# Kernel tuning notes

Hardware: AMD Instinct MI355X
Metric: run time of the kernel (lower is better)

The kernel has to match this reference:

```python
import jax, jax.numpy as jnp
import numpy as np

RPN_BATCHSIZE = 256
RPN_FG_FRACTION = 0.5
NEG_OVERLAP = 0.3
POS_OVERLAP = 0.7
STRIDE = 16
ALLOWED_BORDER = 0.0


def _whctrs(a):
    w = a[2] - a[0] + 1.0
    h = a[3] - a[1] + 1.0
    return w, h, a[0] + 0.5 * (w - 1.0), a[1] + 0.5 * (h - 1.0)


def _mkanchors(ws, hs, xc, yc):
    return np.stack([xc - 0.5 * (ws - 1.0), yc - 0.5 * (hs - 1.0),
                     xc + 0.5 * (ws - 1.0), yc + 0.5 * (hs - 1.0)], axis=1)


def _base_anchors(base_size=16, ratios=(0.5, 1.0, 2.0), scales=(8.0, 16.0, 32.0)):
    ratios = np.asarray(ratios, np.float64)
    scales = np.asarray(scales, np.float64)
    base = np.array([1.0, 1.0, base_size, base_size]) - 1.0
    w, h, xc, yc = _whctrs(base)
    size = w * h
    ws = np.round(np.sqrt(size / ratios))
    hs = np.round(ws * ratios)
    ratio_anchors = _mkanchors(ws, hs, xc, yc)
    out = []
    for ra in ratio_anchors:
        w2, h2, xc2, yc2 = _whctrs(ra)
        out.append(_mkanchors(w2 * scales, h2 * scales, xc2, yc2))
    return np.concatenate(out, axis=0).astype(np.float32)  # (9, 4)


def _shift_anchors(rr, cc, stride):
    base = jnp.asarray(_base_anchors())  # (9, 4)
    sx = jnp.arange(rr, dtype=jnp.float32) * stride
    sy = jnp.arange(cc, dtype=jnp.float32) * stride
    SX, SY = jnp.meshgrid(sx, sy)  # 'xy' indexing like keras meshgrid
    shifts = jnp.stack([SX.ravel(), SY.ravel(), SX.ravel(), SY.ravel()], axis=1)
    return (base[None, :, :] + shifts[:, None, :]).reshape(-1, 4)  # (rr*cc*9, 4)


def _overlap(a, b):
    # pairwise IoU with the +1 pixel convention of keras_rcnn.backend.overlap
    area_a = (a[:, 2] - a[:, 0] + 1.0) * (a[:, 3] - a[:, 1] + 1.0)  # (N,)
    area_b = (b[:, 2] - b[:, 0] + 1.0) * (b[:, 3] - b[:, 1] + 1.0)  # (G,)
    iw = jnp.maximum(jnp.minimum(a[:, None, 2], b[None, :, 2]) - jnp.maximum(a[:, None, 0], b[None, :, 0]) + 1.0, 0.0)
    ih = jnp.maximum(jnp.minimum(a[:, None, 3], b[None, :, 3]) - jnp.maximum(a[:, None, 1], b[None, :, 1]) + 1.0, 0.0)
    inter = iw * ih
    return inter / (area_a[:, None] + area_b[None, :] - inter)


def _subsample(labels, target_value, max_count, key):
    # Randomly demote entries with labels == target_value beyond max_count to -1.
    # Replaces the TF shuffle+scatter with a vectorized rank-based selection.
    is_t = labels == target_value
    pri = jnp.where(is_t, jax.random.uniform(key, labels.shape), -1.0)
    order = jnp.argsort(-pri)
    n = labels.shape[0]
    rank = jnp.zeros((n,), jnp.int32).at[order].set(jnp.arange(n, dtype=jnp.int32))
    drop = is_t & (rank >= max_count)
    return jnp.where(drop, -1.0, labels)


def _bbox_transform(ex, gt):
    ew = ex[:, 2] - ex[:, 0] + 1.0
    eh = ex[:, 3] - ex[:, 1] + 1.0
    ecx = ex[:, 0] + 0.5 * ew
    ecy = ex[:, 1] + 0.5 * eh
    gw = gt[:, 2] - gt[:, 0] + 1.0
    gh = gt[:, 3] - gt[:, 1] + 1.0
    gcx = gt[:, 0] + 0.5 * gw
    gcy = gt[:, 1] + 0.5 * gh
    dx = (gcx - ecx) / ew
    dy = (gcy - ecy) / eh
    dw = jnp.log(gw / ew)
    dh = jnp.log(gh / eh)
    return jnp.stack([dx, dy, dw, dh], axis=1)


def _forward(scores, gt_boxes, metadata):
    meta = metadata[0]
    gt = gt_boxes[0]
    rr, cc = scores.shape[1], scores.shape[2]
    anchors = _shift_anchors(rr, cc, STRIDE)
    n = anchors.shape[0]
    iou = _overlap(anchors, gt)  # (N, G), dominant memory traffic
    argmax_inds = jnp.argmax(iou, axis=1)        # best gt per anchor
    max_overlaps = jnp.max(iou, axis=1)
    gt_argmax_inds = jnp.argmax(iou, axis=0)     # best anchor per gt
    labels = jnp.full((n,), -1.0, jnp.float32)
    labels = jnp.where(max_overlaps < NEG_OVERLAP, 0.0, labels)
    # unique+scatter_add in the original just sets those positions to 1
    labels = labels.at[gt_argmax_inds].set(1.0)
    labels = jnp.where(max_overlaps >= POS_OVERLAP, 1.0, labels)
    kpos, kneg = jax.random.split(jax.random.key(42))
    num_fg = int(RPN_FG_FRACTION * RPN_BATCHSIZE)
    labels = _subsample(labels, 1.0, num_fg, kpos)
    num_bg = RPN_BATCHSIZE - jnp.sum(labels == 1.0)
    labels = _subsample(labels, 0.0, num_bg, kneg)
    gt_sel = gt[argmax_inds]  # (N, 4)
    targets = _bbox_transform(anchors, gt_sel)
    inside = ((anchors[:, 0] >= -ALLOWED_BORDER) & (anchors[:, 1] >= -ALLOWED_BORDER) &
              (anchors[:, 2] < ALLOWED_BORDER + meta[1]) & (anchors[:, 3] < ALLOWED_BORDER + meta[0]))
    labels = jnp.where(inside, labels, -1.0)
    return labels[None, :], targets[None, :, :]


def setup_inputs() -> dict:
    key = jax.random.key(0)
    k1, k2 = jax.random.split(key)
    rr = cc = 128
    num_anchors = 9
    g = 256
    scores = jnp.zeros((1, rr, cc, 2 * num_anchors), jnp.float32)
    xy1 = jax.random.uniform(k1, (g, 2), jnp.float32) * 1600.0
    wh = 32.0 + jax.random.uniform(k2, (g, 2), jnp.float32) * 416.0
    xy2 = jnp.minimum(xy1 + wh, 2047.0)
    gt_boxes = jnp.concatenate([xy1, xy2], axis=1)[None, :, :]
    metadata = jnp.array([[2048.0, 2048.0, 1.0]], jnp.float32)
    return {"scores": scores, "gt_boxes": gt_boxes, "metadata": metadata}


def reference(scores, gt_boxes, metadata):
    return _forward(scores, gt_boxes, metadata)
```

## Files before the change

### kernel.cpp

```cpp
#include <hip/hip_runtime.h>
#include <stdint.h>

#pragma clang fp contract(off)

#define N_ANCH 147456
#define HALF_N 73728u
#define NG 256
#define NBINS 4096
#define CAND_CAP 4096
#define K_POS 128u
#define RPN_BATCH 256u
#define PARTITIONABLE 1

struct TFOut { uint32_t x0, x1; };

__host__ __device__ constexpr TFOut threefry2x32(uint32_t k0, uint32_t k1,
                                                 uint32_t c0, uint32_t c1) {
  uint32_t ks[3] = {k0, k1, k0 ^ k1 ^ 0x1BD11BDAu};
  uint32_t x0 = c0 + ks[0];
  uint32_t x1 = c1 + ks[1];
  const uint32_t rotA[4] = {13u, 15u, 26u, 6u};
  const uint32_t rotB[4] = {17u, 29u, 16u, 24u};
#pragma unroll
  for (int g = 0; g < 5; ++g) {
#pragma unroll
    for (int r = 0; r < 4; ++r) {
      uint32_t ro = ((g & 1) == 0) ? rotA[r] : rotB[r];
      x0 += x1;
      x1 = (x1 << ro) | (x1 >> (32u - ro));
      x1 ^= x0;
    }
    x0 += ks[(g + 1) % 3];
    x1 += ks[(g + 2) % 3] + (uint32_t)(g + 1);
  }
  return TFOut{x0, x1};
}

#if PARTITIONABLE
constexpr TFOut SK0 = threefry2x32(0u, 42u, 0u, 0u);
constexpr TFOut SK1 = threefry2x32(0u, 42u, 0u, 1u);
constexpr uint32_t KPOS0 = SK0.x0, KPOS1 = SK0.x1;
constexpr uint32_t KNEG0 = SK1.x0, KNEG1 = SK1.x1;
#else
constexpr TFOut SA = threefry2x32(0u, 42u, 0u, 2u);
constexpr TFOut SB = threefry2x32(0u, 42u, 1u, 3u);
constexpr uint32_t KPOS0 = SA.x0, KPOS1 = SB.x0;
constexpr uint32_t KNEG0 = SA.x1, KNEG1 = SB.x1;
#endif

__device__ __forceinline__ uint32_t rand_m23(uint32_t k0, uint32_t k1, uint32_t i) {
#if PARTITIONABLE
  TFOut o = threefry2x32(k0, k1, 0u, i);
  return (o.x0 ^ o.x1) >> 9;
#else
  uint32_t lo = (i < HALF_N) ? i : i - HALF_N;
  TFOut o = threefry2x32(k0, k1, lo, lo + HALF_N);
  return ((i < HALF_N) ? o.x0 : o.x1) >> 9;
#endif
}

__device__ const float c_base[9][4] = {
  { -84.f,  -40.f,  99.f,  55.f}, {-176.f,  -88.f, 191.f, 103.f},
  {-360.f, -184.f, 375.f, 199.f}, { -56.f,  -56.f,  71.f,  71.f},
  {-120.f, -120.f, 135.f, 135.f}, {-248.f, -248.f, 263.f, 263.f},
  { -36.f,  -80.f,  51.f,  95.f}, { -80.f, -168.f,  95.f, 183.f},
  {-168.f, -344.f, 183.f, 359.f}
};

__device__ __forceinline__ void anchor_coords(int a, float* x1, float* y1,
                                              float* x2, float* y2) {
  int b = a % 9;
  int cell = a / 9;
  float sx = (float)((cell & 127) << 4);
  float sy = (float)((cell >> 7) << 4);
  *x1 = c_base[b][0] + sx;
  *y1 = c_base[b][1] + sy;
  *x2 = c_base[b][2] + sx;
  *y2 = c_base[b][3] + sy;
}

__global__ __launch_bounds__(256) void k_anchor(const float* __restrict__ gt,
                                                float* __restrict__ labels,
                                                float* __restrict__ targets) {
  __shared__ float4 s_gt[NG];
  __shared__ float s_area[NG];
  const int tid = threadIdx.x;
  float4 bb = ((const float4*)gt)[tid];
  s_gt[tid] = bb;
  s_area[tid] = (bb.z - bb.x + 1.0f) * (bb.w - bb.y + 1.0f);
  __syncthreads();
  const int a = blockIdx.x * 256 + tid;
  float ax1, ay1, ax2, ay2;
  anchor_coords(a, &ax1, &ay1, &ax2, &ay2);
  const float area_a = (ax2 - ax1 + 1.0f) * (ay2 - ay1 + 1.0f);
  float best = -1.0f;
  int bj = 0;
  for (int j = 0; j < NG; ++j) {
    float4 b = s_gt[j];
    float iw = fminf(ax2, b.z) - fmaxf(ax1, b.x) + 1.0f;
    iw = fmaxf(iw, 0.0f);
    float ih = fminf(ay2, b.w) - fmaxf(ay1, b.y) + 1.0f;
    ih = fmaxf(ih, 0.0f);
    float inter = iw * ih;
    float v = inter / (area_a + s_area[j] - inter);
    if (v > best) { best = v; bj = j; }
  }
  labels[a] = (best >= 0.7f) ? 1.0f : ((best < 0.3f) ? 0.0f : -1.0f);
  float4 g = s_gt[bj];
  float ew = ax2 - ax1 + 1.0f;
  float eh = ay2 - ay1 + 1.0f;
  float ecx = ax1 + 0.5f * ew;
  float ecy = ay1 + 0.5f * eh;
  float gw = g.z - g.x + 1.0f;
  float gh = g.w - g.y + 1.0f;
  float gcx = g.x + 0.5f * gw;
  float gcy = g.y + 0.5f * gh;
  float4 t;
  t.x = (gcx - ecx) / ew;
  t.y = (gcy - ecy) / eh;
  t.z = logf(gw / ew);
  t.w = logf(gh / eh);
  ((float4*)targets)[a] = t;
}

__global__ __launch_bounds__(256) void k_gtbest_sep(const float* __restrict__ gt,
                                                    float* __restrict__ labels) {
  __shared__ unsigned long long s_best[2][9];
  __shared__ unsigned long long s_k[9];
  const int j = blockIdx.x;
  const int tid = threadIdx.x;
  if (tid < 18) s_best[tid / 9][tid % 9] = 0ull;
  __syncthreads();
  float4 b = ((const float4*)gt)[j];
  const int axis = tid >> 7;
  const int p = tid & 127;
  const float shift = (float)(p << 4);
  const float lo = axis ? b.y : b.x;
  const float hi = axis ? b.w : b.z;
#pragma unroll
  for (int k = 0; k < 9; ++k) {
    const float a1 = c_base[k][axis] + shift;
    const float a2 = c_base[k][axis + 2] + shift;
    float ext = fminf(a2, hi) - fmaxf(a1, lo) + 1.0f;
    ext = fmaxf(ext, 0.0f);
    unsigned long long key =
        ((unsigned long long)__float_as_uint(ext) << 7)
      | (unsigned long long)(127 - p);
    atomicMax(&s_best[axis][k], key);
  }
  __syncthreads();
  if (tid < 9) {
    const int k = tid;
    unsigned long long kx = s_best[0][k], ky = s_best[1][k];
    float iw = __uint_as_float((uint32_t)(kx >> 7));
    float ih = __uint_as_float((uint32_t)(ky >> 7));
    int xs = 127 - (int)(kx & 127u);
    int ys = 127 - (int)(ky & 127u);
    float inter = iw * ih;
    float area_a = (c_base[k][2] - c_base[k][0] + 1.0f) *
                   (c_base[k][3] - c_base[k][1] + 1.0f);
    float area_b = (b.z - b.x + 1.0f) * (b.w - b.y + 1.0f);
    float v = inter / (area_a + area_b - inter);
    uint32_t a = (uint32_t)((ys * 128 + xs) * 9 + k);
    s_k[k] = ((unsigned long long)__float_as_uint(v) << 32)
           | (unsigned long long)(0xFFFFFFFFu - a);
  }
  __syncthreads();
  if (tid == 0) {
    unsigned long long best = s_k[0];
#pragma unroll
    for (int k = 1; k < 9; ++k) if (s_k[k] > best) best = s_k[k];
    int besta = (int)(0xFFFFFFFFu - (uint32_t)(best & 0xFFFFFFFFull));
    labels[besta] = 1.0f;
  }
}

__global__ __launch_bounds__(256) void k_hist(const float* __restrict__ labels,
                                              uint32_t* __restrict__ hp,
                                              uint32_t* __restrict__ hn) {
  const int a = blockIdx.x * 256 + threadIdx.x;
  float l = labels[a];
  if (l == 1.0f) {
    atomicAdd(&hp[rand_m23(KPOS0, KPOS1, (uint32_t)a) >> 11], 1u);
  } else if (l == 0.0f) {
    atomicAdd(&hn[rand_m23(KNEG0, KNEG1, (uint32_t)a) >> 11], 1u);
  }
}

__global__ __launch_bounds__(1024) void k_findbin(const uint32_t* __restrict__ hp,
                                                  const uint32_t* __restrict__ hn,
                                                  uint32_t* __restrict__ ctrl) {
  __shared__ uint32_t s_h[NBINS];
  __shared__ uint32_t s_c[64];
  __shared__ uint32_t s_kneg;
  const int tid = threadIdx.x;

  for (int i = tid; i < NBINS; i += 1024) s_h[i] = hp[i];
  __syncthreads();
  if (tid < 64) {
    uint32_t s = 0;
    for (int i = 0; i < 64; ++i) s += s_h[tid * 64 + i];
    s_c[tid] = s;
  }
  __syncthreads();
  if (tid == 0) {
    uint32_t total = 0;
    for (int i = 0; i < 64; ++i) total += s_c[i];
    if (total <= K_POS) {
      ctrl[0] = 0u;
      s_kneg = RPN_BATCH - total;
    } else {
      uint32_t cum = 0; int ch, bb;
      for (ch = 63; ch >= 0; --ch) { if (cum + s_c[ch] >= K_POS) break; cum += s_c[ch]; }
      for (bb = ch * 64 + 63; bb >= ch * 64; --bb) { if (cum + s_h[bb] >= K_POS) break; cum += s_h[bb]; }
      ctrl[0] = 1u; ctrl[1] = (uint32_t)bb; ctrl[2] = K_POS - cum;
      s_kneg = RPN_BATCH - K_POS;
    }
  }
  __syncthreads();
  for (int i = tid; i < NBINS; i += 1024) s_h[i] = hn[i];
  __syncthreads();
  if (tid < 64) {
    uint32_t s = 0;
    for (int i = 0; i < 64; ++i) s += s_h[tid * 64 + i];
    s_c[tid] = s;
  }
  __syncthreads();
  if (tid == 0) {
    uint32_t total = 0;
    for (int i = 0; i < 64; ++i) total += s_c[i];
    uint32_t K = s_kneg;
    if (K == 0u) {
      ctrl[4] = 0u;
      ((unsigned long long*)ctrl)[5] = ~0ull;
    } else if (total <= K) {
      ctrl[4] = 0u;
    } else {
      uint32_t cum = 0; int ch, bb;
      for (ch = 63; ch >= 0; --ch) { if (cum + s_c[ch] >= K) break; cum += s_c[ch]; }
      for (bb = ch * 64 + 63; bb >= ch * 64; --bb) { if (cum + s_h[bb] >= K) break; cum += s_h[bb]; }
      ctrl[4] = 1u; ctrl[5] = (uint32_t)bb; ctrl[6] = K - cum;
    }
  }
}

__global__ __launch_bounds__(256) void k_collect(const float* __restrict__ labels,
                                                 uint32_t* __restrict__ ctrl,
                                                 unsigned long long* __restrict__ cp,
                                                 unsigned long long* __restrict__ cn) {
  const int a = blockIdx.x * 256 + threadIdx.x;
  float l = labels[a];
  if (l == 1.0f) {
    if (ctrl[0]) {
      uint32_t m = rand_m23(KPOS0, KPOS1, (uint32_t)a);
      if ((m >> 11) == ctrl[1]) {
        uint32_t i = atomicAdd(&ctrl[3], 1u);
        if (i < CAND_CAP)
          cp[i] = ((unsigned long long)m << 32) | (unsigned long long)(0xFFFFFFFFu - (uint32_t)a);
      }
    }
  } else if (l == 0.0f) {
    if (ctrl[4]) {
      uint32_t m = rand_m23(KNEG0, KNEG1, (uint32_t)a);
      if ((m >> 11) == ctrl[5]) {
        uint32_t i = atomicAdd(&ctrl[7], 1u);
        if (i < CAND_CAP)
          cn[i] = ((unsigned long long)m << 32) | (unsigned long long)(0xFFFFFFFFu - (uint32_t)a);
      }
    }
  }
}

__global__ __launch_bounds__(1024) void k_cutoff(uint32_t* __restrict__ ctrl,
                                                 const unsigned long long* __restrict__ cp,
                                                 const unsigned long long* __restrict__ cn) {
  __shared__ unsigned long long s_k[CAND_CAP];
  __shared__ unsigned long long s_m[1024];
  const int tid = threadIdx.x;
  for (int phase = 0; phase < 2; ++phase) {
    uint32_t active = ctrl[phase ? 4 : 0];
    if (!active) continue;
    uint32_t c = ctrl[phase ? 7 : 3];
    if (c > CAND_CAP) c = CAND_CAP;
    uint32_t need = ctrl[phase ? 6 : 2];
    const unsigned long long* cand = phase ? cn : cp;
    for (uint32_t i = tid; i < c; i += 1024) s_k[i] = cand[i];
    __syncthreads();
    unsigned long long mymin = ~0ull;
    for (uint32_t i = tid; i < c; i += 1024) {
      unsigned long long k = s_k[i];
      uint32_t r = 0;
      for (uint32_t j = 0; j < c; ++j) r += (s_k[j] > k) ? 1u : 0u;
      if (r < need && k < mymin) mymin = k;
    }
    s_m[tid] = mymin;
    __syncthreads();
    for (int s = 512; s > 0; s >>= 1) {
      if (tid < s) {
        unsigned long long o = s_m[tid + s];
        if (o < s_m[tid]) s_m[tid] = o;
      }
      __syncthreads();
    }
    if (tid == 0) ((unsigned long long*)ctrl)[4 + phase] = s_m[0];
    __syncthreads();
  }
}

__global__ __launch_bounds__(256) void k_apply(float* __restrict__ labels,
                                               const float* __restrict__ meta,
                                               const uint32_t* __restrict__ ctrl) {
  const int a = blockIdx.x * 256 + threadIdx.x;
  float l = labels[a];
  const unsigned long long* cut = (const unsigned long long*)ctrl;
  if (l == 1.0f) {
    unsigned long long key = ((unsigned long long)rand_m23(KPOS0, KPOS1, (uint32_t)a) << 32)
                           | (unsigned long long)(0xFFFFFFFFu - (uint32_t)a);
    if (key < cut[4]) l = -1.0f;
  } else if (l == 0.0f) {
    unsigned long long key = ((unsigned long long)rand_m23(KNEG0, KNEG1, (uint32_t)a) << 32)
                           | (unsigned long long)(0xFFFFFFFFu - (uint32_t)a);
    if (key < cut[5]) l = -1.0f;
  }
  float x1, y1, x2, y2;
  anchor_coords(a, &x1, &y1, &x2, &y2);
  float hh = meta[0], ww = meta[1];
  bool inside = (x1 >= 0.0f) && (y1 >= 0.0f) && (x2 < ww) && (y2 < hh);
  if (!inside) l = -1.0f;
  labels[a] = l;
}

extern "C" void kernel_launch(void* const* d_in, const int* in_sizes, int n_in,
                              void* d_out, int out_size, void* d_ws, size_t ws_size,
                              hipStream_t stream) {
  (void)in_sizes; (void)n_in; (void)out_size; (void)ws_size;
  const float* gt   = (const float*)d_in[1];
  const float* meta = (const float*)d_in[2];
  float* labels  = (float*)d_out;
  float* targets = labels + N_ANCH;

  uint8_t* ws = (uint8_t*)d_ws;
  uint32_t* hp   = (uint32_t*)(ws);
  uint32_t* hn   = (uint32_t*)(ws + 16384);
  uint32_t* ctrl = (uint32_t*)(ws + 32768);
  unsigned long long* cp = (unsigned long long*)(ws + 32896);
  unsigned long long* cn = (unsigned long long*)(ws + 32896 + 32768);

  hipMemsetAsync(d_ws, 0, 32896, stream);
  k_anchor     <<<N_ANCH / 256, 256, 0, stream>>>(gt, labels, targets);
  k_gtbest_sep <<<NG, 256, 0, stream>>>(gt, labels);
  k_hist       <<<N_ANCH / 256, 256, 0, stream>>>(labels, hp, hn);
  k_findbin    <<<1, 1024, 0, stream>>>(hp, hn, ctrl);
  k_collect    <<<N_ANCH / 256, 256, 0, stream>>>(labels, ctrl, cp, cn);
  k_cutoff     <<<1, 1024, 0, stream>>>(ctrl, cp, cn);
  k_apply      <<<N_ANCH / 256, 256, 0, stream>>>(labels, meta, ctrl);
}
```

Baseline: 128.7 us.

## Fuse histogram into anchor kernel and skip IoU division for non-overlapping boxes

Builds the random-key histograms inside the anchor IoU kernel, which removes the separate histogram pass over all labels and one launch. The gt-best kernel now uses atomicExch to promote labels and corrects the histogram counts incrementally. The IoU loop splits the running argmax into four packed-key chains and skips the division when the boxes do not overlap, which cuts the dependency chain and the divide work. The cost is more atomic traffic in the anchor kernel and a check of the tie-breaking semantics: packed keys prefer the lowest index among equal values, which matches the original strict '>' scan.

```diff
diff --git a/kernel.cpp b/kernel.cpp
--- a/kernel.cpp
+++ b/kernel.cpp
@@ -81,7 +81,9 @@
 
 __global__ __launch_bounds__(256) void k_anchor(const float* __restrict__ gt,
                                                 float* __restrict__ labels,
-                                                float* __restrict__ targets) {
+                                                float* __restrict__ targets,
+                                                uint32_t* __restrict__ hp,
+                                                uint32_t* __restrict__ hn) {
   __shared__ float4 s_gt[NG];
   __shared__ float s_area[NG];
   const int tid = threadIdx.x;
@@ -93,19 +95,44 @@
   float ax1, ay1, ax2, ay2;
   anchor_coords(a, &ax1, &ay1, &ax2, &ay2);
   const float area_a = (ax2 - ax1 + 1.0f) * (ay2 - ay1 + 1.0f);
-  float best = -1.0f;
-  int bj = 0;
-  for (int j = 0; j < NG; ++j) {
-    float4 b = s_gt[j];
-    float iw = fminf(ax2, b.z) - fmaxf(ax1, b.x) + 1.0f;
-    iw = fmaxf(iw, 0.0f);
-    float ih = fminf(ay2, b.w) - fmaxf(ay1, b.y) + 1.0f;
-    ih = fmaxf(ih, 0.0f);
-    float inter = iw * ih;
-    float v = inter / (area_a + s_area[j] - inter);
-    if (v > best) { best = v; bj = j; }
-  }
-  labels[a] = (best >= 0.7f) ? 1.0f : ((best < 0.3f) ? 0.0f : -1.0f);
+
+  unsigned long long c0 = 0x00000000FFFFFFFFull;
+  unsigned long long c1 = 0ull, c2 = 0ull, c3 = 0ull;
+#define IOU_STEP(JJ, CH)                                                  \
+  {                                                                       \
+    float4 b = s_gt[(JJ)];                                                \
+    float iw = fminf(ax2, b.z) - fmaxf(ax1, b.x) + 1.0f;                  \
+    float ih = fminf(ay2, b.w) - fmaxf(ay1, b.y) + 1.0f;                  \
+    if (iw > 0.0f && ih > 0.0f) {                                         \
+      float inter = iw * ih;                                              \
+      float v = inter / (area_a + s_area[(JJ)] - inter);                  \
+      unsigned long long key =                                            \
+          ((unsigned long long)__float_as_uint(v) << 32)                  \
+        | (unsigned long long)(0xFFFFFFFFu - (uint32_t)(JJ));             \
+      if (key > CH) CH = key;                                             \
+    }                                                                     \
+  }
+  for (int j = 0; j < NG; j += 4) {
+    IOU_STEP(j + 0, c0)
+    IOU_STEP(j + 1, c1)
+    IOU_STEP(j + 2, c2)
+    IOU_STEP(j + 3, c3)
+  }
+#undef IOU_STEP
+  if (c1 > c0) c0 = c1;
+  if (c2 > c0) c0 = c2;
+  if (c3 > c0) c0 = c3;
+  const float best = __uint_as_float((uint32_t)(c0 >> 32));
+  const int bj = (int)(0xFFFFFFFFu - (uint32_t)c0);
+
+  float l = (best >= 0.7f) ? 1.0f : ((best < 0.3f) ? 0.0f : -1.0f);
+  labels[a] = l;
+  if (l == 1.0f) {
+    atomicAdd(&hp[rand_m23(KPOS0, KPOS1, (uint32_t)a) >> 11], 1u);
+  } else if (l == 0.0f) {
+    atomicAdd(&hn[rand_m23(KNEG0, KNEG1, (uint32_t)a) >> 11], 1u);
+  }
+
   float4 g = s_gt[bj];
   float ew = ax2 - ax1 + 1.0f;
   float eh = ay2 - ay1 + 1.0f;
@@ -124,7 +151,9 @@
 }
 
 __global__ __launch_bounds__(256) void k_gtbest_sep(const float* __restrict__ gt,
-                                                    float* __restrict__ labels) {
+                                                    float* __restrict__ labels,
+                                                    uint32_t* __restrict__ hp,
+                                                    uint32_t* __restrict__ hn) {
   __shared__ unsigned long long s_best[2][9];
   __shared__ unsigned long long s_k[9];
   const int j = blockIdx.x;
@@ -170,20 +199,14 @@
     unsigned long long best = s_k[0];
 #pragma unroll
     for (int k = 1; k < 9; ++k) if (s_k[k] > best) best = s_k[k];
-    int besta = (int)(0xFFFFFFFFu - (uint32_t)(best & 0xFFFFFFFFull));
-    labels[besta] = 1.0f;
-  }
-}
-
-__global__ __launch_bounds__(256) void k_hist(const float* __restrict__ labels,
-                                              uint32_t* __restrict__ hp,
-                                              uint32_t* __restrict__ hn) {
-  const int a = blockIdx.x * 256 + threadIdx.x;
-  float l = labels[a];
-  if (l == 1.0f) {
-    atomicAdd(&hp[rand_m23(KPOS0, KPOS1, (uint32_t)a) >> 11], 1u);
-  } else if (l == 0.0f) {
-    atomicAdd(&hn[rand_m23(KNEG0, KNEG1, (uint32_t)a) >> 11], 1u);
+    uint32_t besta = 0xFFFFFFFFu - (uint32_t)(best & 0xFFFFFFFFull);
+    float old = atomicExch(&labels[besta], 1.0f);
+    if (old == 0.0f) {
+      atomicSub(&hn[rand_m23(KNEG0, KNEG1, besta) >> 11], 1u);
+      atomicAdd(&hp[rand_m23(KPOS0, KPOS1, besta) >> 11], 1u);
+    } else if (old == -1.0f) {
+      atomicAdd(&hp[rand_m23(KPOS0, KPOS1, besta) >> 11], 1u);
+    }
   }
 }
 
@@ -347,9 +370,8 @@
   unsigned long long* cn = (unsigned long long*)(ws + 32896 + 32768);
 
   hipMemsetAsync(d_ws, 0, 32896, stream);
-  k_anchor     <<<N_ANCH / 256, 256, 0, stream>>>(gt, labels, targets);
-  k_gtbest_sep <<<NG, 256, 0, stream>>>(gt, labels);
-  k_hist       <<<N_ANCH / 256, 256, 0, stream>>>(labels, hp, hn);
+  k_anchor     <<<N_ANCH / 256, 256, 0, stream>>>(gt, labels, targets, hp, hn);
+  k_gtbest_sep <<<NG, 256, 0, stream>>>(gt, labels, hp, hn);
   k_findbin    <<<1, 1024, 0, stream>>>(hp, hn, ctrl);
   k_collect    <<<N_ANCH / 256, 256, 0, stream>>>(labels, ctrl, cp, cn);
   k_cutoff     <<<1, 1024, 0, stream>>>(ctrl, cp, cn);
```

Result: faster. 110.1 us (-14.5%).
